# Kernel tuning notes

Hardware: AMD Instinct MI355X
Metric: run time of the kernel (lower is better)

Reference implementation:

```python
import jax, jax.numpy as jnp
import numpy as np

N_HEADS = 16


def setup_inputs() -> dict:
    key = jax.random.key(0)
    k1, k2, k3, k4 = jax.random.split(key, 4)
    B, T, C = 2, 2048, 1024
    x = jax.random.normal(k1, (B, T, C), dtype=jnp.float32)
    scale = 1.0 / np.sqrt(C)
    Wq = jax.random.normal(k2, (C, C), dtype=jnp.float32) * scale
    Wk = jax.random.normal(k3, (C, C), dtype=jnp.float32) * scale
    Wv = jax.random.normal(k4, (C, C), dtype=jnp.float32) * scale
    return {"x": x, "Wq": Wq, "Wk": Wk, "Wv": Wv}


def reference(x, Wq, Wk, Wv):
    B, T, C = x.shape
    H = N_HEADS
    Dh = C // H
    # Faithful to original: direct view of (B,T,C) -> (B,H,T,Dh) (no transpose)
    q = (x @ Wq.T).reshape(B, H, T, Dh)
    k = (x @ Wk.T).reshape(B, H, T, Dh)
    v = (x @ Wv.T).reshape(B, H, T, Dh)
    scores = jnp.einsum('bhqd,bhkd->bhqk', q, k) * (1.0 / (Dh ** 0.5))
    mask = jnp.tril(jnp.ones((T, T), dtype=bool))  # causal mask
    scores = jnp.where(mask, scores, -jnp.inf)
    att = jax.nn.softmax(scores, axis=-1)
    out = jnp.einsum('bhqk,bhkd->bhqd', att, v)
    return out.reshape(B, T, C)
```

## Files before the change

### kernel.cpp

```cpp
#include <hip/hip_runtime.h>
#include <hip/hip_bf16.h>
#include <stdint.h>

#define AS1 __attribute__((address_space(1)))
#define AS3 __attribute__((address_space(3)))

typedef __bf16 bf16x8 __attribute__((ext_vector_type(8)));
typedef float  f32x4  __attribute__((ext_vector_type(4)));
typedef unsigned short ushort8v __attribute__((ext_vector_type(8)));
typedef unsigned short ushort4v __attribute__((ext_vector_type(4)));
typedef short short8v __attribute__((ext_vector_type(8)));
typedef short short4v __attribute__((ext_vector_type(4)));

__device__ __forceinline__ unsigned short f2bf(float f) {
    unsigned int u = __float_as_uint(f);
    u += 0x7fffu + ((u >> 16) & 1u);
    return (unsigned short)(u >> 16);
}
__device__ __forceinline__ unsigned int pk2bf(float a, float b) {
    __hip_bfloat162 h = __float22bfloat162_rn(make_float2(a, b));
    unsigned int u;
    __builtin_memcpy(&u, &h, 4);
    return u;
}
__device__ __forceinline__ void g2lds16(const void* gp, void* lp) {
    __builtin_amdgcn_global_load_lds((AS1 void*)gp, (AS3 void*)lp, 16, 0, 0);
}
#define E2(x) __builtin_amdgcn_exp2f(x)

__global__ __launch_bounds__(256) void cast_all(const float* __restrict__ x,
                                                const float* __restrict__ w0,
                                                const float* __restrict__ w1,
                                                const float* __restrict__ w2,
                                                unsigned short* __restrict__ xb,
                                                unsigned short* __restrict__ wc) {
    int id = blockIdx.x;
    const float* s;
    unsigned short* d;
    int base;
    if (id < 4096) { s = x; d = xb; base = id; }
    else {
        int z = (id - 4096) >> 10;
        s = (z == 0) ? w0 : (z == 1) ? w1 : w2;
        d = wc + (size_t)z * 1048576;
        base = (id - 4096) & 1023;
    }
    int i = (base * 256 + threadIdx.x) * 4;
    float4 v = *(const float4*)(s + i);
    ushort4v o = { f2bf(v.x), f2bf(v.y), f2bf(v.z), f2bf(v.w) };
    *(ushort4v*)(d + i) = o;
}

__global__ __launch_bounds__(256) void gemm_qkv(const unsigned short* __restrict__ X,
                                                const unsigned short* __restrict__ W,
                                                unsigned short* __restrict__ QKV) {
    const int K = 1024, N = 1024;
    const int z = blockIdx.z;
    const unsigned short* A = X;
    const unsigned short* B = W + (size_t)z * (1024 * 1024);
    unsigned short* C = QKV + (size_t)z * (4096 * 1024);
    const float qs = (z == 0) ? 0.18033688011112042f : 1.0f;

    const int m0 = blockIdx.y * 128;
    const int n0 = blockIdx.x * 128;

    __shared__ unsigned short As[128 * 32];
    __shared__ unsigned short Bs[128 * 32];

    const int t = threadIdx.x;
    const int w = t >> 6;
    const int l = t & 63;
    const int wm = (w >> 1) * 64;
    const int wn = (w & 1) * 64;
    const int cl = l & 15;
    const int quad = l >> 4;

    const int srow = w * 16 + (l >> 2);
    const int scol = (l & 3) * 8;

    f32x4 acc[4][4] = {};

    for (int k0 = 0; k0 < K; k0 += 32) {
        g2lds16(A + (size_t)(m0 + srow) * K + k0 + scol,      As + w * 512);
        g2lds16(A + (size_t)(m0 + 64 + srow) * K + k0 + scol, As + 2048 + w * 512);
        g2lds16(B + (size_t)(n0 + srow) * K + k0 + scol,      Bs + w * 512);
        g2lds16(B + (size_t)(n0 + 64 + srow) * K + k0 + scol, Bs + 2048 + w * 512);
        __syncthreads();

        bf16x8 af[4], bfr[4];
        #pragma unroll
        for (int i = 0; i < 4; ++i)
            af[i] = *(const bf16x8*)(As + (wm + i * 16 + cl) * 32 + quad * 8);
        #pragma unroll
        for (int j = 0; j < 4; ++j)
            bfr[j] = *(const bf16x8*)(Bs + (wn + j * 16 + cl) * 32 + quad * 8);
        #pragma unroll
        for (int i = 0; i < 4; ++i)
            #pragma unroll
            for (int j = 0; j < 4; ++j)
                acc[i][j] = __builtin_amdgcn_mfma_f32_16x16x32_bf16(af[i], bfr[j], acc[i][j], 0, 0, 0);
        __syncthreads();
    }

    #pragma unroll
    for (int i = 0; i < 4; ++i) {
        #pragma unroll
        for (int r = 0; r < 4; ++r) {
            size_t row = (size_t)(m0 + wm + i * 16 + quad * 4 + r);
            #pragma unroll
            for (int j = 0; j < 4; ++j)
                C[row * N + (n0 + wn + j * 16 + cl)] = f2bf(acc[i][j][r] * qs);
        }
    }
}

__global__ __launch_bounds__(256) void vtrans(const unsigned short* __restrict__ Vn,
                                              unsigned short* __restrict__ V3) {
    const int bh = blockIdx.y;
    const int T0 = blockIdx.x * 128;
    __shared__ unsigned short L[128 * 72];
    const int t = threadIdx.x;

    const unsigned short* src = Vn + (size_t)bh * 131072 + (size_t)T0 * 64;
    #pragma unroll
    for (int p = 0; p < 4; ++p) {
        int r = p * 32 + (t >> 3), c = (t & 7) * 8;
        *(ushort8v*)(L + r * 72 + c) = *(const ushort8v*)(src + (size_t)r * 64 + c);
    }
    __syncthreads();
    unsigned short* dst = V3 + (size_t)bh * 131072 + (size_t)(T0 >> 4) * 1024;
    #pragma unroll
    for (int p = 0; p < 2; ++p) {
        int item = p * 256 + t;
        int kb = item >> 6, cl = (item >> 2) & 15, qk = item & 3;
        ushort8v a, b;
        #pragma unroll
        for (int u = 0; u < 8; ++u) {
            int dt = u >> 2, j = u & 3;
            a[u] = L[(kb * 16 + qk * 4 + j) * 72 + dt * 16 + cl];
            b[u] = L[(kb * 16 + qk * 4 + j) * 72 + (dt + 2) * 16 + cl];
        }
        unsigned short* dp = dst + kb * 1024 + cl * 64 + qk * 16;
        *(ushort8v*)(dp) = a;
        *(ushort8v*)(dp + 8) = b;
    }
}

__global__ __launch_bounds__(1024) void attn(const unsigned short* __restrict__ QK,
                                             const unsigned short* __restrict__ V3,
                                             float* __restrict__ Out) {
    const int id = blockIdx.x;
    const int bh = (id & 7) * 4 + ((id >> 3) & 3);
    const int pp = id >> 5;
    const int t = threadIdx.x;
    const int w = t >> 6;
    const int l = t & 63;
    const int cl = l & 15;
    const int quad = l >> 4;
    const int c7 = cl & 7;
    const int wl = w & 7;

    const size_t bhoff = (size_t)bh * 131072;
    const unsigned short* Qb = QK + bhoff;
    const unsigned short* Kb = QK + (size_t)4194304 + bhoff;
    const unsigned short* Vb = V3 + bhoff;
    float* Ob = Out + bhoff;

    __shared__ unsigned short KVs[2][8192];

    const int sg = t;
    const int kO = (sg >> 3) * 64 + (((sg & 7) ^ ((sg >> 3) & 7)) * 8);
    const int wg = sg & 63;
    const int vO = (sg >> 6) * 512 + ((wg ^ ((wg >> 3) & 7)) * 8);
    const int lB = wl * 512;

    const int oK0 = cl * 64 + (((quad)     ^ c7) * 8);
    const int oK1 = cl * 64 + (((quad + 4) ^ c7) * 8);
    const int oV0 = cl * 64 + (((quad * 2)     ^ c7) * 8);
    const int oV1 = cl * 64 + (((quad * 2 + 1) ^ c7) * 8);

    const int mrel = (wl & 3) * 16 + cl;

    const int bb = (w < 8) ? pp : (15 - pp);
    const int nchB = 2 * (15 - pp) + 2;
    const int myLast = 2 * bb + (wl >> 2);
    const int m0w = bb * 128 + wl * 16;

    bf16x8 qf0, qf1;
    {
        const unsigned short* qa = Qb + (size_t)(m0w + cl) * 64 + quad * 8;
        qf0 = *(const bf16x8*)(qa);
        qf1 = *(const bf16x8*)(qa + 32);
    }

    f32x4 o[4] = {};
    float lps = 0.f;

    if (w < 8) {
        unsigned short* s = &KVs[0][0];
        g2lds16(Kb + kO, s + lB);
        g2lds16(Vb + vO, s + 4096 + lB);
    }

    for (int c = 0; c < nchB; ++c) {
        __syncthreads();
        if (w < 8 && c + 1 < nchB) {
            unsigned short* s = &KVs[(c + 1) & 1][0];
            g2lds16(Kb + (size_t)(c + 1) * 4096 + kO, s + lB);
            g2lds16(Vb + (size_t)(c + 1) * 4096 + vO, s + 4096 + lB);
        }
        if (c > myLast) continue;
        const unsigned short* Kl = &KVs[c & 1][0];
        const unsigned short* Vl = Kl + 4096;
        const bool masked = (c == myLast);

        bf16x8 kf0[4], kf1[4];
        #pragma unroll
        for (int kt = 0; kt < 4; ++kt) {
            kf0[kt] = *(const bf16x8*)(Kl + kt * 1024 + oK0);
            kf1[kt] = *(const bf16x8*)(Kl + kt * 1024 + oK1);
        }
        f32x4 st[4] = {};
        __builtin_amdgcn_s_setprio(1);
        #pragma unroll
        for (int kt = 0; kt < 4; ++kt) {
            st[kt] = __builtin_amdgcn_mfma_f32_16x16x32_bf16(kf0[kt], qf0, st[kt], 0, 0, 0);
            st[kt] = __builtin_amdgcn_mfma_f32_16x16x32_bf16(kf1[kt], qf1, st[kt], 0, 0, 0);
        }
        __builtin_amdgcn_s_setprio(0);

        short4v pb[4];
        #pragma unroll
        for (int kt = 0; kt < 4; ++kt) {
            float p0, p1, p2, p3;
            if (masked) {
                const int lk = kt * 16 + quad * 4;
                p0 = (lk     <= mrel) ? E2(st[kt][0]) : 0.f;
                p1 = (lk + 1 <= mrel) ? E2(st[kt][1]) : 0.f;
                p2 = (lk + 2 <= mrel) ? E2(st[kt][2]) : 0.f;
                p3 = (lk + 3 <= mrel) ? E2(st[kt][3]) : 0.f;
            } else {
                p0 = E2(st[kt][0]);
                p1 = E2(st[kt][1]);
                p2 = E2(st[kt][2]);
                p3 = E2(st[kt][3]);
            }
            lps += (p0 + p1) + (p2 + p3);
            uint2 u = { pk2bf(p0, p1), pk2bf(p2, p3) };
            short4v pv;
            __builtin_memcpy(&pv, &u, 8);
            pb[kt] = pv;
        }

        __builtin_amdgcn_s_setprio(1);
        #pragma unroll
        for (int kt = 0; kt < 4; ++kt) {
            short8v v0 = *(const short8v*)(Vl + kt * 1024 + oV0);
            short8v v1 = *(const short8v*)(Vl + kt * 1024 + oV1);
            short4v a0 = __builtin_shufflevector(v0, v0, 0, 1, 2, 3);
            short4v a1 = __builtin_shufflevector(v0, v0, 4, 5, 6, 7);
            short4v a2 = __builtin_shufflevector(v1, v1, 0, 1, 2, 3);
            short4v a3 = __builtin_shufflevector(v1, v1, 4, 5, 6, 7);
            o[0] = __builtin_amdgcn_mfma_f32_16x16x16bf16_1k(a0, pb[kt], o[0], 0, 0, 0);
            o[1] = __builtin_amdgcn_mfma_f32_16x16x16bf16_1k(a1, pb[kt], o[1], 0, 0, 0);
            o[2] = __builtin_amdgcn_mfma_f32_16x16x16bf16_1k(a2, pb[kt], o[2], 0, 0, 0);
            o[3] = __builtin_amdgcn_mfma_f32_16x16x16bf16_1k(a3, pb[kt], o[3], 0, 0, 0);
        }
        __builtin_amdgcn_s_setprio(0);
    }

    lps += __shfl_xor(lps, 16);
    lps += __shfl_xor(lps, 32);
    const float inv = 1.0f / lps;
    #pragma unroll
    for (int dt = 0; dt < 4; ++dt) {
        f32x4 r = o[dt];
        r[0] *= inv; r[1] *= inv; r[2] *= inv; r[3] *= inv;
        *(f32x4*)(Ob + (size_t)(m0w + cl) * 64 + dt * 16 + quad * 4) = r;
    }
}

extern "C" void kernel_launch(void* const* d_in, const int* in_sizes, int n_in,
                              void* d_out, int out_size, void* d_ws, size_t ws_size,
                              hipStream_t stream) {
    const float* x  = (const float*)d_in[0];
    const float* Wq = (const float*)d_in[1];
    const float* Wk = (const float*)d_in[2];
    const float* Wv = (const float*)d_in[3];
    float* out = (float*)d_out;

    unsigned short* xb  = (unsigned short*)d_ws;
    unsigned short* wc  = xb + (size_t)4096 * 1024;
    unsigned short* qkv = wc + (size_t)3 * 1024 * 1024;
    unsigned short* vt  = qkv + (size_t)3 * 4096 * 1024;

    hipLaunchKernelGGL(cast_all, dim3(7168), dim3(256), 0, stream, x, Wq, Wk, Wv, xb, wc);
    hipLaunchKernelGGL(gemm_qkv, dim3(8, 32, 3), dim3(256), 0, stream, xb, wc, qkv);
    hipLaunchKernelGGL(vtrans, dim3(16, 32), dim3(256), 0, stream, qkv + (size_t)2 * 4096 * 1024, vt);
    hipLaunchKernelGGL(attn, dim3(256), dim3(1024), 0, stream, qkv, vt, out);
}
```

Baseline: 150.1 us.

## Split attention into 256-thread blocks, one 64-row query tile each, heaviest first

The attention kernel changes from 256 blocks of 1024 threads, each pairing two 128-row query tiles to balance the causal workload, to 1024 blocks of 256 threads, each handling a single 64-row query tile. Blocks are ordered so the longest causal tiles launch first, and every thread now issues two K and two V async loads per chunk. The aim is better occupancy (launch bounds 256,4) and finer scheduling granularity, with no idle waves waiting on shared chunks. The cost is that K/V chunks are reloaded by more blocks, which raises L2 traffic, and the in-block load pairing is lost.

```diff
diff --git a/kernel.cpp b/kernel.cpp
--- a/kernel.cpp
+++ b/kernel.cpp
@@ -146,19 +146,18 @@
     }
 }
 
-__global__ __launch_bounds__(1024) void attn(const unsigned short* __restrict__ QK,
-                                             const unsigned short* __restrict__ V3,
-                                             float* __restrict__ Out) {
+__global__ __launch_bounds__(256, 4) void attn(const unsigned short* __restrict__ QK,
+                                               const unsigned short* __restrict__ V3,
+                                               float* __restrict__ Out) {
     const int id = blockIdx.x;
-    const int bh = (id & 7) * 4 + ((id >> 3) & 3);
-    const int pp = id >> 5;
+    const int bh = id & 31;
+    const int bb = 31 - (id >> 5);
     const int t = threadIdx.x;
     const int w = t >> 6;
     const int l = t & 63;
     const int cl = l & 15;
     const int quad = l >> 4;
     const int c7 = cl & 7;
-    const int wl = w & 7;
 
     const size_t bhoff = (size_t)bh * 131072;
     const unsigned short* Qb = QK + bhoff;
@@ -168,23 +167,24 @@
 
     __shared__ unsigned short KVs[2][8192];
 
-    const int sg = t;
-    const int kO = (sg >> 3) * 64 + (((sg & 7) ^ ((sg >> 3) & 7)) * 8);
-    const int wg = sg & 63;
-    const int vO = (sg >> 6) * 512 + ((wg ^ ((wg >> 3) & 7)) * 8);
-    const int lB = wl * 512;
+    const int g2 = t + 256;
+    const int kO1 = (t >> 3) * 64 + (((t & 7) ^ ((t >> 3) & 7)) * 8);
+    const int kO2 = (g2 >> 3) * 64 + (((g2 & 7) ^ ((g2 >> 3) & 7)) * 8);
+    const int wg1 = t & 63;
+    const int wg2 = g2 & 63;
+    const int vO1 = (t >> 6) * 512 + ((wg1 ^ ((wg1 >> 3) & 7)) * 8);
+    const int vO2 = (g2 >> 6) * 512 + ((wg2 ^ ((wg2 >> 3) & 7)) * 8);
+    const int lB1 = w * 512;
+    const int lB2 = 2048 + w * 512;
 
     const int oK0 = cl * 64 + (((quad)     ^ c7) * 8);
     const int oK1 = cl * 64 + (((quad + 4) ^ c7) * 8);
     const int oV0 = cl * 64 + (((quad * 2)     ^ c7) * 8);
     const int oV1 = cl * 64 + (((quad * 2 + 1) ^ c7) * 8);
 
-    const int mrel = (wl & 3) * 16 + cl;
-
-    const int bb = (w < 8) ? pp : (15 - pp);
-    const int nchB = 2 * (15 - pp) + 2;
-    const int myLast = 2 * bb + (wl >> 2);
-    const int m0w = bb * 128 + wl * 16;
+    const int mrel = w * 16 + cl;
+    const int nch = bb + 1;
+    const int m0w = bb * 64 + w * 16;
 
     bf16x8 qf0, qf1;
     {
@@ -196,23 +196,27 @@
     f32x4 o[4] = {};
     float lps = 0.f;
 
-    if (w < 8) {
+    {
         unsigned short* s = &KVs[0][0];
-        g2lds16(Kb + kO, s + lB);
-        g2lds16(Vb + vO, s + 4096 + lB);
-    }
-
-    for (int c = 0; c < nchB; ++c) {
+        g2lds16(Kb + kO1, s + lB1);
+        g2lds16(Kb + kO2, s + lB2);
+        g2lds16(Vb + vO1, s + 4096 + lB1);
+        g2lds16(Vb + vO2, s + 4096 + lB2);
+    }
+
+    for (int c = 0; c < nch; ++c) {
         __syncthreads();
-        if (w < 8 && c + 1 < nchB) {
+        if (c + 1 < nch) {
             unsigned short* s = &KVs[(c + 1) & 1][0];
-            g2lds16(Kb + (size_t)(c + 1) * 4096 + kO, s + lB);
-            g2lds16(Vb + (size_t)(c + 1) * 4096 + vO, s + 4096 + lB);
-        }
-        if (c > myLast) continue;
+            const size_t off = (size_t)(c + 1) * 4096;
+            g2lds16(Kb + off + kO1, s + lB1);
+            g2lds16(Kb + off + kO2, s + lB2);
+            g2lds16(Vb + off + vO1, s + 4096 + lB1);
+            g2lds16(Vb + off + vO2, s + 4096 + lB2);
+        }
         const unsigned short* Kl = &KVs[c & 1][0];
         const unsigned short* Vl = Kl + 4096;
-        const bool masked = (c == myLast);
+        const bool masked = (c == bb);
 
         bf16x8 kf0[4], kf1[4];
         #pragma unroll
@@ -297,5 +301,5 @@
     hipLaunchKernelGGL(cast_all, dim3(7168), dim3(256), 0, stream, x, Wq, Wk, Wv, xb, wc);
     hipLaunchKernelGGL(gemm_qkv, dim3(8, 32, 3), dim3(256), 0, stream, xb, wc, qkv);
     hipLaunchKernelGGL(vtrans, dim3(16, 32), dim3(256), 0, stream, qkv + (size_t)2 * 4096 * 1024, vt);
-    hipLaunchKernelGGL(attn, dim3(256), dim3(1024), 0, stream, qkv, vt, out);
-}
+    hipLaunchKernelGGL(attn, dim3(1024), dim3(256), 0, stream, qkv, vt, out);
+}
```

After: 147.4 us. About the same (-1.8%).
